# Performance work log

Hardware: AMD Instinct MI355X
Metric: run time of the kernel (lower is better)

Reference implementation:

```python
import jax, jax.numpy as jnp
import numpy as np

B, S, H, I, G = 2, 1024, 1024, 4096, 8


def setup_inputs() -> dict:
    key = jax.random.key(0)
    k1, k2, k3, k4 = jax.random.split(key, 4)
    # kaiming-style scaled init (scale matters only for numerics, not math)
    hidden_states = jax.random.normal(k1, (B, S, H), dtype=jnp.float32)
    WG = jax.random.normal(k2, (H, G), dtype=jnp.float32) * (1.0 / np.sqrt(H))
    Wi = jax.random.normal(k3, (G, H, I), dtype=jnp.float32) * (1.0 / np.sqrt(H))
    down = jax.random.normal(k4, (I, H), dtype=jnp.float32) * (1.0 / np.sqrt(I))
    return {"hidden_states": hidden_states, "WG": WG, "Wi": Wi, "down": down, "topk": 2}


def topk_sigmoid(gate, k):
    # gate: [B,S,G] -> sigmoid gated scores masked to top-k per token
    _, idx = jax.lax.top_k(gate, k)                       # idx: [B,S,k]
    mask = (idx[..., None] == jnp.arange(gate.shape[-1])).any(axis=-2)  # [B,S,G] bool
    return jax.nn.sigmoid(gate) * mask


def reference(hidden_states, WG, Wi, down, topk):
    gate = hidden_states @ WG                             # [B,S,G]
    g = topk_sigmoid(gate, topk)                          # [B,S,G]
    # dense contraction over all groups (faithful to original einsum)
    up = jnp.einsum('bse,bsg,geo->bso', hidden_states, g, Wi)  # [B,S,I]
    act = jnp.square(jax.nn.relu(up))                     # ReLU^2
    return act @ down                                     # [B,S,H]
```

## Files before the change

### kernel.cpp

```cpp
#include <hip/hip_runtime.h>
#include <hip/hip_bf16.h>

typedef unsigned short u16;
typedef short short8_t __attribute__((ext_vector_type(8)));
typedef float f32x4 __attribute__((ext_vector_type(4)));

#define GLOBAL_AS(p) ((const __attribute__((address_space(1))) void*)(p))
#define LDS_AS(p)    ((__attribute__((address_space(3))) void*)(p))

__device__ __forceinline__ u16 f2bf(float f) {
    union { float f; unsigned int u; } x;
    x.f = f;
    unsigned int r = x.u + 0x7fffu + ((x.u >> 16) & 1u);
    return (u16)(r >> 16);
}

#define M_NMT   0
#define M_TE    2
#define M_TB    42
#define M_PAIR  96
#define M_RTOK  4192
#define M_RW    9312

__global__ __launch_bounds__(64) void gate_topk_kernel(
    const float* __restrict__ h, const float* __restrict__ wg, float* __restrict__ w) {
    const int t = blockIdx.x;
    const int lane = threadIdx.x;
    float acc[8];
#pragma unroll
    for (int g = 0; g < 8; ++g) acc[g] = 0.f;
    for (int e = lane; e < 1024; e += 64) {
        float hv = h[(size_t)t * 1024 + e];
        float4 r0 = *(const float4*)&wg[e * 8];
        float4 r1 = *(const float4*)&wg[e * 8 + 4];
        acc[0] += hv * r0.x; acc[1] += hv * r0.y; acc[2] += hv * r0.z; acc[3] += hv * r0.w;
        acc[4] += hv * r1.x; acc[5] += hv * r1.y; acc[6] += hv * r1.z; acc[7] += hv * r1.w;
    }
#pragma unroll
    for (int off = 32; off > 0; off >>= 1) {
#pragma unroll
        for (int g = 0; g < 8; ++g) acc[g] += __shfl_down(acc[g], off);
    }
    if (lane == 0) {
        int i1 = 0;
        for (int g = 1; g < 8; ++g) if (acc[g] > acc[i1]) i1 = g;
        int i2 = -1;
        for (int g = 0; g < 8; ++g) {
            if (g == i1) continue;
            if (i2 < 0 || acc[g] > acc[i2]) i2 = g;
        }
#pragma unroll
        for (int g = 0; g < 8; ++g) {
            float v = (g == i1 || g == i2) ? (1.f / (1.f + __expf(-acc[g]))) : 0.f;
            w[t * 8 + g] = v;
        }
    }
}

__global__ __launch_bounds__(256) void scan_kernel(
    const float* __restrict__ w, int* __restrict__ meta) {
    __shared__ int cnt[8], pos[8];
    const int tid = threadIdx.x;
    if (tid < 8) cnt[tid] = 0;
    __syncthreads();
    for (int t = tid; t < 2048; t += 256) {
#pragma unroll
        for (int g = 0; g < 8; ++g)
            if (w[t * 8 + g] > 0.f) atomicAdd(&cnt[g], 1);
    }
    __syncthreads();
    if (tid == 0) {
        int base = 0, mt = 0;
        for (int e = 0; e < 8; ++e) {
            pos[e] = base;
            int nt = (cnt[e] + 127) >> 7;
            for (int k = 0; k < nt; ++k) { meta[M_TE + mt] = e; meta[M_TB + mt] = base + k * 128; ++mt; }
            base += nt << 7;
        }
        meta[M_NMT] = mt;
        meta[1] = base;
    }
    __syncthreads();
    for (int i = tid; i < 5120; i += 256) meta[M_RTOK + i] = -1;
    __syncthreads();
    float* row_w = (float*)&meta[M_RW];
    for (int t = tid; t < 2048; t += 256) {
        int slot = 0;
#pragma unroll
        for (int g = 0; g < 8; ++g) {
            float wv = w[t * 8 + g];
            if (wv > 0.f) {
                int p = atomicAdd(&pos[g], 1);
                meta[M_RTOK + p] = t;
                row_w[p] = wv;
                meta[M_PAIR + t * 2 + slot] = p;
                ++slot;
            }
        }
    }
}

__global__ __launch_bounds__(256) void gather_a_kernel(
    const float* __restrict__ h, const int* __restrict__ meta, u16* __restrict__ A) {
    const int row = blockIdx.x;
    const int tid = threadIdx.x;
    const int tok = meta[M_RTOK + row];
    u16* dst = A + (size_t)row * 1024;
    if (tok < 0) {
        uint2 z; z.x = 0u; z.y = 0u;
        ((uint2*)dst)[tid] = z;
        return;
    }
    const float wv = ((const float*)&meta[M_RW])[row];
    float4 v = ((const float4*)(h + (size_t)tok * 1024))[tid];
    u16 o[4] = { f2bf(v.x * wv), f2bf(v.y * wv), f2bf(v.z * wv), f2bf(v.w * wv) };
    ((uint2*)dst)[tid] = *(const uint2*)o;
}

__global__ __launch_bounds__(256) void gemm1_sparse_kernel(
    const u16* __restrict__ A, const float* __restrict__ Wi,
    float* __restrict__ up, const int* __restrict__ meta) {
    const int mt = blockIdx.y;
    if (mt >= meta[M_NMT]) return;
    const int e = meta[M_TE + mt];
    const int base = meta[M_TB + mt];
    const int n0 = blockIdx.x * 128;
    const int K = 1024, N = 4096;
    const float* Bm = Wi + (size_t)e * K * N;

    __shared__ short a_tile[128 * 64];
    __shared__ short b_tile[128 * 64];
    const int tid = threadIdx.x;
    const int lane = tid & 63;
    const int wave = tid >> 6;
    const int wm = (wave >> 1) * 64;
    const int wn = (wave & 1) * 64;
    const int r = lane & 15;
    const int quad = lane >> 4;
    const int rowin = lane >> 3;
    const int achk = ((lane & 7) ^ (rowin & 7)) * 8;
    const int aldst = (lane & 7) * 8;

    const int bidx_n = tid & 127;
    const int bidx_k8 = tid >> 7;

    const f32x4 vzero = {0.f, 0.f, 0.f, 0.f};
    f32x4 acc[4][4];
#pragma unroll
    for (int i = 0; i < 4; ++i)
#pragma unroll
        for (int j = 0; j < 4; ++j) acc[i][j] = vzero;

    float bv[4][8];
#pragma unroll
    for (int cb = 0; cb < 4; ++cb) {
        const float* bp = Bm + (size_t)((bidx_k8 + cb * 2) * 8) * N + n0 + bidx_n;
#pragma unroll
        for (int kk = 0; kk < 8; ++kk) bv[cb][kk] = bp[(size_t)kk * N];
    }

    for (int kb = 0; kb < K; kb += 64) {
#pragma unroll
        for (int it = 0; it < 4; ++it) {
            int row = wave * 8 + it * 32 + rowin;
            const u16* ga = A + (size_t)(base + row) * K + kb + achk;
            __builtin_amdgcn_global_load_lds(GLOBAL_AS(ga), LDS_AS(&a_tile[row * 64 + aldst]), 16, 0, 0);
        }
#pragma unroll
        for (int cb = 0; cb < 4; ++cb) {
            int bk8 = bidx_k8 + cb * 2;
            u16 bc[8];
#pragma unroll
            for (int kk = 0; kk < 8; ++kk) bc[kk] = f2bf(bv[cb][kk]);
            *(short8_t*)&b_tile[bidx_n * 64 + ((bk8 ^ (bidx_n & 7)) * 8)] = *(const short8_t*)bc;
        }
        __syncthreads();

        if (kb + 64 < K) {
#pragma unroll
            for (int cb = 0; cb < 4; ++cb) {
                const float* bp = Bm + (size_t)(kb + 64 + (bidx_k8 + cb * 2) * 8) * N + n0 + bidx_n;
#pragma unroll
                for (int kk = 0; kk < 8; ++kk) bv[cb][kk] = bp[(size_t)kk * N];
            }
        }

#pragma unroll
        for (int ks = 0; ks < 2; ++ks) {
            const int cp = ((ks * 4 + quad) ^ (r & 7)) * 8;
            short8_t af[4], bfr[4];
#pragma unroll
            for (int i = 0; i < 4; ++i)
                af[i] = *(const short8_t*)&a_tile[(wm + i * 16 + r) * 64 + cp];
#pragma unroll
            for (int j = 0; j < 4; ++j)
                bfr[j] = *(const short8_t*)&b_tile[(wn + j * 16 + r) * 64 + cp];
#pragma unroll
            for (int i = 0; i < 4; ++i)
#pragma unroll
                for (int j = 0; j < 4; ++j)
                    acc[i][j] = __builtin_amdgcn_mfma_f32_16x16x32_bf16(af[i], bfr[j], acc[i][j], 0, 0, 0);
        }
        __syncthreads();
    }
#pragma unroll
    for (int i = 0; i < 4; ++i)
#pragma unroll
        for (int j = 0; j < 4; ++j)
#pragma unroll
            for (int reg = 0; reg < 4; ++reg) {
                int cr = base + wm + i * 16 + quad * 4 + reg;
                int cc = n0 + wn + j * 16 + r;
                up[(size_t)cr * N + cc] = acc[i][j][reg];
            }
}

__global__ __launch_bounds__(256) void combine_kernel(
    const float* __restrict__ up, const int* __restrict__ meta, u16* __restrict__ act) {
    const int t = blockIdx.x;
    const int tid = threadIdx.x;
    const int p0 = meta[M_PAIR + t * 2];
    const int p1 = meta[M_PAIR + t * 2 + 1];
    const float* r0 = up + (size_t)p0 * 4096;
    const float* r1 = up + (size_t)p1 * 4096;
    u16* dst = act + (size_t)t * 4096;
#pragma unroll
    for (int it = 0; it < 4; ++it) {
        int i = (tid + it * 256) * 4;
        float4 a = *(const float4*)&r0[i];
        float4 b = *(const float4*)&r1[i];
        float s0 = a.x + b.x, s1 = a.y + b.y, s2 = a.z + b.z, s3 = a.w + b.w;
        s0 = s0 > 0.f ? s0 * s0 : 0.f;
        s1 = s1 > 0.f ? s1 * s1 : 0.f;
        s2 = s2 > 0.f ? s2 * s2 : 0.f;
        s3 = s3 > 0.f ? s3 * s3 : 0.f;
        u16 o[4] = { f2bf(s0), f2bf(s1), f2bf(s2), f2bf(s3) };
        *(uint2*)&dst[i] = *(const uint2*)o;
    }
}

__global__ __launch_bounds__(256) void transpose_cvt_kernel(
    const float* __restrict__ in, u16* __restrict__ out, int R, int C) {
    __shared__ u16 tile[64][65];
    const int rt = blockIdx.y * 64;
    const int ct = blockIdx.x * 64;
    const int tid = threadIdx.x;
#pragma unroll
    for (int it = 0; it < 2; ++it) {
        int r = (tid >> 3) + it * 32;
        int c8 = (tid & 7) * 8;
        const float* ip = &in[(size_t)(rt + r) * C + ct + c8];
        float4 v0 = *(const float4*)ip;
        float4 v1 = *(const float4*)(ip + 4);
        tile[c8 + 0][r] = f2bf(v0.x); tile[c8 + 1][r] = f2bf(v0.y);
        tile[c8 + 2][r] = f2bf(v0.z); tile[c8 + 3][r] = f2bf(v0.w);
        tile[c8 + 4][r] = f2bf(v1.x); tile[c8 + 5][r] = f2bf(v1.y);
        tile[c8 + 6][r] = f2bf(v1.z); tile[c8 + 7][r] = f2bf(v1.w);
    }
    __syncthreads();
#pragma unroll
    for (int it = 0; it < 2; ++it) {
        int c = (tid >> 3) + it * 32;
        int r8 = (tid & 7) * 8;
        u16 tmp[8];
#pragma unroll
        for (int j = 0; j < 8; ++j) tmp[j] = tile[c][r8 + j];
        *(uint4*)&out[(size_t)(ct + c) * R + rt + r8] = *(const uint4*)tmp;
    }
}

template <int BM, int WROWS, int WCOLS>
__global__ __launch_bounds__(256) void gemm_tn_kernel(
    const u16* __restrict__ X, const u16* __restrict__ Y, float* __restrict__ Cout,
    int M, int N, int K) {
    constexpr int WM = BM / WROWS;
    constexpr int WN = 128 / WCOLS;
    constexpr int FI = WM / 16;
    constexpr int FJ = WN / 16;
    __shared__ short a_tile[BM * 64];
    __shared__ short b_tile[128 * 64];
    const int tid = threadIdx.x;
    const int lane = tid & 63;
    const int wave = tid >> 6;

    const int Nt = gridDim.x, Mt = gridDim.y;
    const int lid = blockIdx.y * Nt + blockIdx.x;
    const int xcd = lid & 7;
    const int p = lid >> 3;
    const int n_tile = xcd * (Nt >> 3) + p / Mt;
    const int m_tile = p % Mt;
    const int m0 = m_tile * BM;
    const int n0 = n_tile * 128;

    const int wm = (wave / WCOLS) * WM;
    const int wn = (wave % WCOLS) * WN;
    const int rowin = lane >> 3;
    const int achk = ((lane & 7) ^ (rowin & 7)) * 8;
    const int aldst = (lane & 7) * 8;
    const int r = lane & 15;
    const int quad = lane >> 4;

    const f32x4 vzero = {0.f, 0.f, 0.f, 0.f};
    f32x4 acc[FI][FJ];
#pragma unroll
    for (int i = 0; i < FI; ++i)
#pragma unroll
        for (int j = 0; j < FJ; ++j) acc[i][j] = vzero;

    for (int kb = 0; kb < K; kb += 64) {
#pragma unroll
        for (int it = 0; it < BM / 32; ++it) {
            int row = wave * 8 + it * 32 + rowin;
            const u16* ga = X + (size_t)(m0 + row) * K + kb + achk;
            __builtin_amdgcn_global_load_lds(GLOBAL_AS(ga), LDS_AS(&a_tile[row * 64 + aldst]), 16, 0, 0);
        }
#pragma unroll
        for (int it = 0; it < 4; ++it) {
            int row = wave * 8 + it * 32 + rowin;
            const u16* gb = Y + (size_t)(n0 + row) * K + kb + achk;
            __builtin_amdgcn_global_load_lds(GLOBAL_AS(gb), LDS_AS(&b_tile[row * 64 + aldst]), 16, 0, 0);
        }
        __syncthreads();
#pragma unroll
        for (int ks = 0; ks < 2; ++ks) {
            const int cp = ((ks * 4 + quad) ^ (r & 7)) * 8;
            short8_t af[FI], bfr[FJ];
#pragma unroll
            for (int i = 0; i < FI; ++i)
                af[i] = *(const short8_t*)&a_tile[(wm + i * 16 + r) * 64 + cp];
#pragma unroll
            for (int j = 0; j < FJ; ++j)
                bfr[j] = *(const short8_t*)&b_tile[(wn + j * 16 + r) * 64 + cp];
#pragma unroll
            for (int i = 0; i < FI; ++i)
#pragma unroll
                for (int j = 0; j < FJ; ++j)
                    acc[i][j] = __builtin_amdgcn_mfma_f32_16x16x32_bf16(af[i], bfr[j], acc[i][j], 0, 0, 0);
        }
        __syncthreads();
    }
#pragma unroll
    for (int i = 0; i < FI; ++i)
#pragma unroll
        for (int j = 0; j < FJ; ++j)
#pragma unroll
            for (int reg = 0; reg < 4; ++reg) {
                int cr = m0 + wm + i * 16 + quad * 4 + reg;
                int cc = n0 + wn + j * 16 + r;
                Cout[(size_t)cr * N + cc] = acc[i][j][reg];
            }
}

extern "C" void kernel_launch(void* const* d_in, const int* in_sizes, int n_in,
                              void* d_out, int out_size, void* d_ws, size_t ws_size,
                              hipStream_t stream) {
    const float* h    = (const float*)d_in[0];
    const float* WG   = (const float*)d_in[1];
    const float* Wi   = (const float*)d_in[2];
    const float* down = (const float*)d_in[3];
    float* out = (float*)d_out;

    const int T = 2048, H = 1024, I = 4096;

    char* ws = (char*)d_ws;
    float* w_gate = (float*)(ws);
    int*   meta   = (int*)(ws + 65536);
    u16*   Arow   = (u16*)(ws + 131072);
    float* up     = (float*)(ws + 131072 + 10485760);
    u16*   act    = (u16*)(ws + 131072 + 10485760 + 83886080);
    u16*   downT  = (u16*)(ws + 131072 + 10485760 + 83886080 + 16777216);

    gate_topk_kernel<<<T, 64, 0, stream>>>(h, WG, w_gate);
    scan_kernel<<<1, 256, 0, stream>>>(w_gate, meta);
    gather_a_kernel<<<5120, 256, 0, stream>>>(h, meta, Arow);

    gemm1_sparse_kernel<<<dim3(32, 40), 256, 0, stream>>>(Arow, Wi, up, meta);

    combine_kernel<<<T, 256, 0, stream>>>(up, meta, act);

    transpose_cvt_kernel<<<dim3(H / 64, I / 64), 256, 0, stream>>>(down, downT, I, H);
    gemm_tn_kernel<64, 1, 4><<<dim3(H / 128, T / 64), 256, 0, stream>>>(
        act, downT, out, T, H, I);
}
```

Measured before the change: 373.4 us.

## Split-K second GEMM reading fp32 weights directly, widen scan, restage B loads

The down-projection no longer runs a separate transpose-and-convert pass. A new NN GEMM reads the fp32 down matrix directly, converts it in registers, uses 128x128 tiles and a 4-way split-K (512 blocks), and writes partial sums into the reused up buffer; a reduce kernel then adds the four partials. The scan kernel moves to 1024 threads. The gemm1 B prefetch now loads half the tile ahead and the other half inside the iteration, using inline asm loads. This removes one kernel and the extra weight round trip, at the cost of extra partial-sum traffic, a reduce pass, and more register pressure and exposed latency in gemm1.

Result: faster. 340.7 us (-8.8%).

```diff
diff --git a/kernel.cpp b/kernel.cpp
--- a/kernel.cpp
+++ b/kernel.cpp
@@ -57,13 +57,13 @@
     }
 }
 
-__global__ __launch_bounds__(256) void scan_kernel(
+__global__ __launch_bounds__(1024) void scan_kernel(
     const float* __restrict__ w, int* __restrict__ meta) {
     __shared__ int cnt[8], pos[8];
     const int tid = threadIdx.x;
     if (tid < 8) cnt[tid] = 0;
     __syncthreads();
-    for (int t = tid; t < 2048; t += 256) {
+    for (int t = tid; t < 2048; t += 1024) {
 #pragma unroll
         for (int g = 0; g < 8; ++g)
             if (w[t * 8 + g] > 0.f) atomicAdd(&cnt[g], 1);
@@ -81,10 +81,10 @@
         meta[1] = base;
     }
     __syncthreads();
-    for (int i = tid; i < 5120; i += 256) meta[M_RTOK + i] = -1;
+    for (int i = tid; i < 5120; i += 1024) meta[M_RTOK + i] = -1;
     __syncthreads();
     float* row_w = (float*)&meta[M_RW];
-    for (int t = tid; t < 2048; t += 256) {
+    for (int t = tid; t < 2048; t += 1024) {
         int slot = 0;
 #pragma unroll
         for (int g = 0; g < 8; ++g) {
@@ -151,12 +151,14 @@
 #pragma unroll
         for (int j = 0; j < 4; ++j) acc[i][j] = vzero;
 
-    float bv[4][8];
-#pragma unroll
-    for (int cb = 0; cb < 4; ++cb) {
+    float bvp[2][8];
+    float bvt[2][8];
+
+#pragma unroll
+    for (int cb = 0; cb < 2; ++cb) {
         const float* bp = Bm + (size_t)((bidx_k8 + cb * 2) * 8) * N + n0 + bidx_n;
 #pragma unroll
-        for (int kk = 0; kk < 8; ++kk) bv[cb][kk] = bp[(size_t)kk * N];
+        for (int kk = 0; kk < 8; ++kk) bvp[cb][kk] = bp[(size_t)kk * N];
     }
 
     for (int kb = 0; kb < K; kb += 64) {
@@ -167,21 +169,38 @@
             __builtin_amdgcn_global_load_lds(GLOBAL_AS(ga), LDS_AS(&a_tile[row * 64 + aldst]), 16, 0, 0);
         }
 #pragma unroll
-        for (int cb = 0; cb < 4; ++cb) {
+        for (int cb = 0; cb < 2; ++cb) {
             int bk8 = bidx_k8 + cb * 2;
             u16 bc[8];
 #pragma unroll
-            for (int kk = 0; kk < 8; ++kk) bc[kk] = f2bf(bv[cb][kk]);
+            for (int kk = 0; kk < 8; ++kk) bc[kk] = f2bf(bvp[cb][kk]);
             *(short8_t*)&b_tile[bidx_n * 64 + ((bk8 ^ (bidx_n & 7)) * 8)] = *(const short8_t*)bc;
         }
+#pragma unroll
+        for (int cb = 0; cb < 2; ++cb) {
+            const float* bp = Bm + (size_t)(kb + (bidx_k8 + (cb + 2) * 2) * 8) * N + n0 + bidx_n;
+#pragma unroll
+            for (int kk = 0; kk < 8; ++kk) bvt[cb][kk] = bp[(size_t)kk * N];
+        }
+#pragma unroll
+        for (int cb = 0; cb < 2; ++cb) {
+            int bk8 = bidx_k8 + (cb + 2) * 2;
+            u16 bc[8];
+#pragma unroll
+            for (int kk = 0; kk < 8; ++kk) bc[kk] = f2bf(bvt[cb][kk]);
+            *(short8_t*)&b_tile[bidx_n * 64 + ((bk8 ^ (bidx_n & 7)) * 8)] = *(const short8_t*)bc;
+        }
         __syncthreads();
 
         if (kb + 64 < K) {
 #pragma unroll
-            for (int cb = 0; cb < 4; ++cb) {
+            for (int cb = 0; cb < 2; ++cb) {
                 const float* bp = Bm + (size_t)(kb + 64 + (bidx_k8 + cb * 2) * 8) * N + n0 + bidx_n;
 #pragma unroll
-                for (int kk = 0; kk < 8; ++kk) bv[cb][kk] = bp[(size_t)kk * N];
+                for (int kk = 0; kk < 8; ++kk) {
+                    asm volatile("global_load_dword %0, %1, off"
+                                 : "=v"(bvp[cb][kk]) : "v"(bp + (size_t)kk * N));
+                }
             }
         }
 
@@ -239,116 +258,121 @@
     }
 }
 
-__global__ __launch_bounds__(256) void transpose_cvt_kernel(
-    const float* __restrict__ in, u16* __restrict__ out, int R, int C) {
-    __shared__ u16 tile[64][65];
-    const int rt = blockIdx.y * 64;
-    const int ct = blockIdx.x * 64;
-    const int tid = threadIdx.x;
-#pragma unroll
-    for (int it = 0; it < 2; ++it) {
-        int r = (tid >> 3) + it * 32;
-        int c8 = (tid & 7) * 8;
-        const float* ip = &in[(size_t)(rt + r) * C + ct + c8];
-        float4 v0 = *(const float4*)ip;
-        float4 v1 = *(const float4*)(ip + 4);
-        tile[c8 + 0][r] = f2bf(v0.x); tile[c8 + 1][r] = f2bf(v0.y);
-        tile[c8 + 2][r] = f2bf(v0.z); tile[c8 + 3][r] = f2bf(v0.w);
-        tile[c8 + 4][r] = f2bf(v1.x); tile[c8 + 5][r] = f2bf(v1.y);
-        tile[c8 + 6][r] = f2bf(v1.z); tile[c8 + 7][r] = f2bf(v1.w);
-    }
-    __syncthreads();
-#pragma unroll
-    for (int it = 0; it < 2; ++it) {
-        int c = (tid >> 3) + it * 32;
-        int r8 = (tid & 7) * 8;
-        u16 tmp[8];
-#pragma unroll
-        for (int j = 0; j < 8; ++j) tmp[j] = tile[c][r8 + j];
-        *(uint4*)&out[(size_t)(ct + c) * R + rt + r8] = *(const uint4*)tmp;
-    }
-}
-
-template <int BM, int WROWS, int WCOLS>
-__global__ __launch_bounds__(256) void gemm_tn_kernel(
-    const u16* __restrict__ X, const u16* __restrict__ Y, float* __restrict__ Cout,
-    int M, int N, int K) {
-    constexpr int WM = BM / WROWS;
-    constexpr int WN = 128 / WCOLS;
-    constexpr int FI = WM / 16;
-    constexpr int FJ = WN / 16;
-    __shared__ short a_tile[BM * 64];
+__global__ __launch_bounds__(256) void gemm2_nn_kernel(
+    const u16* __restrict__ X, const float* __restrict__ B, float* __restrict__ Pout) {
+    const int M = 2048, N = 1024, K = 4096;
+    const int lid = blockIdx.y * 8 + blockIdx.x;
+    const int xcd = lid & 7;
+    const int p = lid >> 3;
+    const int m_tile = xcd * 2 + (p & 1);
+    const int n_tile = p >> 1;
+    const int m0 = m_tile * 128;
+    const int n0 = n_tile * 128;
+    const int kb0 = blockIdx.z * 1024;
+
+    __shared__ short a_tile[128 * 64];
     __shared__ short b_tile[128 * 64];
     const int tid = threadIdx.x;
     const int lane = tid & 63;
     const int wave = tid >> 6;
-
-    const int Nt = gridDim.x, Mt = gridDim.y;
-    const int lid = blockIdx.y * Nt + blockIdx.x;
-    const int xcd = lid & 7;
-    const int p = lid >> 3;
-    const int n_tile = xcd * (Nt >> 3) + p / Mt;
-    const int m_tile = p % Mt;
-    const int m0 = m_tile * BM;
-    const int n0 = n_tile * 128;
-
-    const int wm = (wave / WCOLS) * WM;
-    const int wn = (wave % WCOLS) * WN;
+    const int wm = (wave >> 1) * 64;
+    const int wn = (wave & 1) * 64;
+    const int r = lane & 15;
+    const int quad = lane >> 4;
     const int rowin = lane >> 3;
     const int achk = ((lane & 7) ^ (rowin & 7)) * 8;
     const int aldst = (lane & 7) * 8;
-    const int r = lane & 15;
-    const int quad = lane >> 4;
+
+    const int bidx_n = tid & 127;
+    const int bidx_k8 = tid >> 7;
 
     const f32x4 vzero = {0.f, 0.f, 0.f, 0.f};
-    f32x4 acc[FI][FJ];
-#pragma unroll
-    for (int i = 0; i < FI; ++i)
-#pragma unroll
-        for (int j = 0; j < FJ; ++j) acc[i][j] = vzero;
-
-    for (int kb = 0; kb < K; kb += 64) {
-#pragma unroll
-        for (int it = 0; it < BM / 32; ++it) {
-            int row = wave * 8 + it * 32 + rowin;
-            const u16* ga = X + (size_t)(m0 + row) * K + kb + achk;
-            __builtin_amdgcn_global_load_lds(GLOBAL_AS(ga), LDS_AS(&a_tile[row * 64 + aldst]), 16, 0, 0);
-        }
+    f32x4 acc[4][4];
+#pragma unroll
+    for (int i = 0; i < 4; ++i)
+#pragma unroll
+        for (int j = 0; j < 4; ++j) acc[i][j] = vzero;
+
+    float bv[4][8];
+#pragma unroll
+    for (int cb = 0; cb < 4; ++cb) {
+        const float* bp = B + (size_t)(kb0 + (bidx_k8 + cb * 2) * 8) * N + n0 + bidx_n;
+#pragma unroll
+        for (int kk = 0; kk < 8; ++kk) bv[cb][kk] = bp[(size_t)kk * N];
+    }
+
+    for (int kb = 0; kb < 1024; kb += 64) {
 #pragma unroll
         for (int it = 0; it < 4; ++it) {
             int row = wave * 8 + it * 32 + rowin;
-            const u16* gb = Y + (size_t)(n0 + row) * K + kb + achk;
-            __builtin_amdgcn_global_load_lds(GLOBAL_AS(gb), LDS_AS(&b_tile[row * 64 + aldst]), 16, 0, 0);
+            const u16* ga = X + (size_t)(m0 + row) * K + kb0 + kb + achk;
+            __builtin_amdgcn_global_load_lds(GLOBAL_AS(ga), LDS_AS(&a_tile[row * 64 + aldst]), 16, 0, 0);
+        }
+#pragma unroll
+        for (int cb = 0; cb < 4; ++cb) {
+            int bk8 = bidx_k8 + cb * 2;
+            u16 bc[8];
+#pragma unroll
+            for (int kk = 0; kk < 8; ++kk) bc[kk] = f2bf(bv[cb][kk]);
+            *(short8_t*)&b_tile[bidx_n * 64 + ((bk8 ^ (bidx_n & 7)) * 8)] = *(const short8_t*)bc;
         }
         __syncthreads();
+
+        if (kb + 64 < 1024) {
+#pragma unroll
+            for (int cb = 0; cb < 4; ++cb) {
+                const float* bp = B + (size_t)(kb0 + kb + 64 + (bidx_k8 + cb * 2) * 8) * N + n0 + bidx_n;
+#pragma unroll
+                for (int kk = 0; kk < 8; ++kk) bv[cb][kk] = bp[(size_t)kk * N];
+            }
+        }
+
 #pragma unroll
         for (int ks = 0; ks < 2; ++ks) {
             const int cp = ((ks * 4 + quad) ^ (r & 7)) * 8;
-            short8_t af[FI], bfr[FJ];
-#pragma unroll
-            for (int i = 0; i < FI; ++i)
+            short8_t af[4], bfr[4];
+#pragma unroll
+            for (int i = 0; i < 4; ++i)
                 af[i] = *(const short8_t*)&a_tile[(wm + i * 16 + r) * 64 + cp];
 #pragma unroll
-            for (int j = 0; j < FJ; ++j)
+            for (int j = 0; j < 4; ++j)
                 bfr[j] = *(const short8_t*)&b_tile[(wn + j * 16 + r) * 64 + cp];
 #pragma unroll
-            for (int i = 0; i < FI; ++i)
-#pragma unroll
-                for (int j = 0; j < FJ; ++j)
+            for (int i = 0; i < 4; ++i)
+#pragma unroll
+                for (int j = 0; j < 4; ++j)
                     acc[i][j] = __builtin_amdgcn_mfma_f32_16x16x32_bf16(af[i], bfr[j], acc[i][j], 0, 0, 0);
         }
         __syncthreads();
     }
-#pragma unroll
-    for (int i = 0; i < FI; ++i)
-#pragma unroll
-        for (int j = 0; j < FJ; ++j)
+
+    float* Co = Pout + (size_t)blockIdx.z * M * N;
+#pragma unroll
+    for (int i = 0; i < 4; ++i)
+#pragma unroll
+        for (int j = 0; j < 4; ++j)
 #pragma unroll
             for (int reg = 0; reg < 4; ++reg) {
                 int cr = m0 + wm + i * 16 + quad * 4 + reg;
                 int cc = n0 + wn + j * 16 + r;
-                Cout[(size_t)cr * N + cc] = acc[i][j][reg];
+                Co[(size_t)cr * N + cc] = acc[i][j][reg];
             }
+}
+
+__global__ __launch_bounds__(256) void reduce4_kernel(
+    const float* __restrict__ P, float* __restrict__ out) {
+    const size_t S = (size_t)2048 * 1024;
+    size_t i = ((size_t)blockIdx.x * 256 + threadIdx.x) * 4;
+    float4 a = *(const float4*)&P[i];
+    float4 b = *(const float4*)&P[S + i];
+    float4 c = *(const float4*)&P[2 * S + i];
+    float4 d = *(const float4*)&P[3 * S + i];
+    float4 o;
+    o.x = (a.x + b.x) + (c.x + d.x);
+    o.y = (a.y + b.y) + (c.y + d.y);
+    o.z = (a.z + b.z) + (c.z + d.z);
+    o.w = (a.w + b.w) + (c.w + d.w);
+    *(float4*)&out[i] = o;
 }
 
 extern "C" void kernel_launch(void* const* d_in, const int* in_sizes, int n_in,
@@ -360,7 +384,7 @@
     const float* down = (const float*)d_in[3];
     float* out = (float*)d_out;
 
-    const int T = 2048, H = 1024, I = 4096;
+    const int T = 2048;
 
     char* ws = (char*)d_ws;
     float* w_gate = (float*)(ws);
@@ -368,17 +392,16 @@
     u16*   Arow   = (u16*)(ws + 131072);
     float* up     = (float*)(ws + 131072 + 10485760);
     u16*   act    = (u16*)(ws + 131072 + 10485760 + 83886080);
-    u16*   downT  = (u16*)(ws + 131072 + 10485760 + 83886080 + 16777216);
+    float* part   = up;
 
     gate_topk_kernel<<<T, 64, 0, stream>>>(h, WG, w_gate);
-    scan_kernel<<<1, 256, 0, stream>>>(w_gate, meta);
+    scan_kernel<<<1, 1024, 0, stream>>>(w_gate, meta);
     gather_a_kernel<<<5120, 256, 0, stream>>>(h, meta, Arow);
 
     gemm1_sparse_kernel<<<dim3(32, 40), 256, 0, stream>>>(Arow, Wi, up, meta);
 
     combine_kernel<<<T, 256, 0, stream>>>(up, meta, act);
 
-    transpose_cvt_kernel<<<dim3(H / 64, I / 64), 256, 0, stream>>>(down, downT, I, H);
-    gemm_tn_kernel<64, 1, 4><<<dim3(H / 128, T / 64), 256, 0, stream>>>(
-        act, downT, out, T, H, I);
-}
+    gemm2_nn_kernel<<<dim3(8, 16, 4), 256, 0, stream>>>(act, down, part);
+    reduce4_kernel<<<(T * 1024) / 1024, 256, 0, stream>>>(part, out);
+}
```
